# Kernel optimization log

Measured on AMD Instinct MI355X. Metric: run time of the kernel, lower is better.

The kernel has to match this reference:

```python
import jax, jax.numpy as jnp
import numpy as np


def _consts(n_fft):
    # Static index/twiddle tables, mirroring FastIMDCT4.__init__ (numpy, host-side).
    N4 = n_fft // 4
    k = np.arange(N4)
    pre0 = 2 * k                       # even taps
    pre1 = n_fft // 2 - 1 - 2 * k      # reversed odd taps
    tw = np.exp(-2j * np.pi / n_fft * (k.astype(np.float32) + 0.125)).astype(np.complex64)
    # post-FFT de-interleave index (length n_fft, values in [0, n_fft//2))
    idx = np.empty(n_fft, np.int64)
    idx[0:n_fft // 2:2] = np.arange(0, n_fft // 2, 2)
    idx[1:n_fft // 2:2] = np.arange(n_fft // 2 - 1, 0, -2)
    idx[n_fft // 2:] = idx[:n_fft // 2][::-1]
    post = np.roll(idx, -n_fft // 4)
    # sign pattern folded into the window
    sign = np.ones(n_fft, np.float64)
    sign[1::2] *= -1.0
    sign[:n_fft // 4] *= -1.0
    sign = np.roll(sign, -n_fft // 4)
    return pre0, pre1, tw, post, sign


def setup_inputs() -> dict:
    key = jax.random.key(0)
    B, T, n_fft, hop = 32, 1024, 2048, 1024
    signal = jax.random.normal(key, (B, T, n_fft // 2), dtype=jnp.float32)
    window = jnp.ones((n_fft,), dtype=jnp.float32)  # raw window (module default: ones)
    return {"signal": signal, "window": window, "n_fft": n_fft, "hop_length": hop}


def reference(signal, window, n_fft, hop_length):
    pre0, pre1, tw, post, sign = _consts(n_fft)
    # combined window: 4 * sign * window / n_fft (module precomputes this in __init__)
    win = (4.0 * jnp.asarray(sign, jnp.float32) * window / n_fft)
    # pre-twiddle gather -> complex [B, T, n_fft//4]
    c = signal[..., pre0] + 1j * signal[..., pre1]
    twj = jnp.asarray(tw)
    c = twj * c
    c = jnp.fft.fft(c, axis=-1)
    c = twj * c
    B, T = c.shape[0], c.shape[1]
    # interleave real/imag -> [B, T, n_fft//2], then post gather -> [B, T, n_fft]
    inter = jnp.stack([jnp.real(c), jnp.imag(c)], axis=-1).reshape(B, T, n_fft // 2)
    frames = win * inter[..., post]            # [B, T, n_fft]
    # overlap-add fold (F.fold with kernel (1, n_fft), stride (1, hop))
    out_len = (T - 1) * hop_length + n_fft
    pos = (np.arange(T)[:, None] * hop_length + np.arange(n_fft)[None, :]).reshape(-1)
    out = jnp.zeros((B, out_len), frames.dtype).at[:, pos].add(frames.reshape(B, -1))
    # center=True trimming
    out = out[:, n_fft // 2: -(n_fft // 2)]
    return out[:, None, None, :]               # [B, 1, 1, (T-1)*hop], matches fold output layout
```

## Files before the change

### kernel.cpp

```cpp
#include <hip/hip_runtime.h>


#define CHUNKS 1023

__device__ __forceinline__ float2 cmul(float2 a, float2 b) {
    return make_float2(a.x * b.x - a.y * b.y, a.x * b.y + a.y * b.x);
}
__device__ __forceinline__ float2 cadd(float2 a, float2 b) {
    return make_float2(a.x + b.x, a.y + b.y);
}
__device__ __forceinline__ float2 csub(float2 a, float2 b) {
    return make_float2(a.x - b.x, a.y - b.y);
}
__device__ __forceinline__ float2 twid(float rev) {
    return make_float2(__builtin_amdgcn_cosf(rev), __builtin_amdgcn_sinf(rev));
}

__device__ __forceinline__ void postmap(int m, int& p, float& sgn) {
    bool even = ((m & 1) == 0);
    if (m < 512)       p = even ? (m + 512)  : (512 - m);
    else if (m < 1536) p = even ? (m - 511)  : (1535 - m);
    else               p = even ? (m - 1536) : (2560 - m);
    float s1 = even ? 1.0f : -1.0f;
    sgn = (m < 1536) ? s1 : -s1;
}

__device__ __forceinline__ int brev3(int r) {
    return ((r & 1) << 2) | (r & 2) | ((r >> 2) & 1);
}

__device__ __forceinline__ void fft_frame(const float* __restrict__ row, int lane,
                                          float* __restrict__ planes) {
    const float2* row2 = (const float2*)row;
    const int rlane = (int)(__brev((unsigned)lane) >> 26);

    float2 v[8];
    #pragma unroll
    for (int r = 0; r < 8; ++r) v[r] = row2[64 * r + rlane];

    float2 c[8];
    #pragma unroll
    for (int r = 0; r < 8; ++r) {
        float im = __shfl_xor(v[7 - r].y, 63);
        int k = 64 * r + rlane;
        float rev = -((float)k + 0.125f) * (1.0f / 2048.0f);
        c[r] = cmul(twid(rev), make_float2(v[r].x, im));
    }

    const float RH = 0.70710678118654752f;
    {
        float2 u0 = c[0], u1 = c[1], u2 = c[2], u3 = c[3];
        float2 l0 = c[4], l1 = c[5], l2 = c[6], l3 = c[7];
        float2 t1 = csub(u1, l1), t2 = csub(u2, l2), t3 = csub(u3, l3);
        c[0] = cadd(u0, l0); c[4] = csub(u0, l0);
        c[1] = cadd(u1, l1); c[5] = cmul(make_float2(RH, -RH), t1);
        c[2] = cadd(u2, l2); c[6] = make_float2(t2.y, -t2.x);
        c[3] = cadd(u3, l3); c[7] = cmul(make_float2(-RH, -RH), t3);
    }
    #pragma unroll
    for (int b = 0; b < 8; b += 4) {
        float2 u0 = c[b], u1 = c[b + 1], d0 = c[b + 2], d1 = c[b + 3];
        float2 t = csub(u1, d1);
        c[b] = cadd(u0, d0);
        c[b + 2] = csub(u0, d0);
        c[b + 1] = cadd(u1, d1);
        c[b + 3] = make_float2(t.y, -t.x);
    }
    #pragma unroll
    for (int b = 0; b < 8; b += 2) {
        float2 u = c[b], d = c[b + 1];
        c[b] = cadd(u, d); c[b + 1] = csub(u, d);
    }

    #pragma unroll
    for (int r = 1; r < 8; ++r) {
        int k1 = brev3(r);
        float rev = -(float)(rlane * k1) * (1.0f / 512.0f);
        c[r] = cmul(twid(rev), c[r]);
    }

    #pragma unroll
    for (int s = 1; s <= 6; ++s) {
        const int half = 1 << (s - 1);
        const bool hi = (lane & half) != 0;
        float rev = -(float)(lane & (half - 1)) / (float)(1 << s);
        float2 w = twid(rev);
        #pragma unroll
        for (int r = 0; r < 8; ++r) {
            float ox = __shfl_xor(c[r].x, half);
            float oy = __shfl_xor(c[r].y, half);
            float2 oth = make_float2(ox, oy);
            if (s == 1) {
                c[r] = hi ? csub(oth, c[r]) : cadd(c[r], oth);
            } else {
                float2 t = cmul(w, hi ? c[r] : oth);
                c[r] = hi ? csub(oth, t) : cadd(c[r], t);
            }
        }
    }

    float2 d[8];
    #pragma unroll
    for (int j = 0; j < 8; ++j) {
        int r = brev3(j);
        int k = j + 8 * lane;
        float rev = -((float)k + 0.125f) * (1.0f / 2048.0f);
        d[j] = cmul(twid(rev), c[r]);
    }
    float4 r0 = make_float4(d[0].x, d[1].x, d[2].x, d[3].x);
    float4 r1 = make_float4(d[4].x, d[5].x, d[6].x, d[7].x);
    float4 i0 = make_float4(d[0].y, d[1].y, d[2].y, d[3].y);
    float4 i1 = make_float4(d[4].y, d[5].y, d[6].y, d[7].y);
    *(float4*)(planes + 8 * lane)           = r0;
    *(float4*)(planes + 8 * lane + 4)       = r1;
    *(float4*)(planes + 512 + 8 * lane)     = i0;
    *(float4*)(planes + 512 + 8 * lane + 4) = i1;
}

__global__ __launch_bounds__(256) void imdct_kernel(
        const float* __restrict__ signal,
        const float* __restrict__ window,
        float* __restrict__ out) {
    __shared__ float lds[4][2][2 * 512];

    const int tid = threadIdx.x;
    const int lane = tid & 63;
    const int w = tid >> 6;

    const int bid = blockIdx.x;
    const int nb = (bid & 7) * 1023 + (bid >> 3);
    const int chunk = nb * 4 + w;
    const int b = chunk / CHUNKS;
    const int q = chunk - b * CHUNKS;

    const float* base = signal + (size_t)(b * 1024 + q) * 1024;
    fft_frame(base,        lane, &lds[w][0][0]);
    fft_frame(base + 1024, lane, &lds[w][1][0]);

    const float* f0 = &lds[w][0][0];
    const float* f1 = &lds[w][1][0];
    float* orow = out + (size_t)b * (CHUNKS * 1024) + (size_t)q * 1024;

    #pragma unroll
    for (int it = 0; it < 4; ++it) {
        const int rbase = 256 * it + 4 * lane;
        float4 w_hi = *(const float4*)(window + 1024 + rbase);
        float4 w_lo = *(const float4*)(window + rbase);
        const float* whp = &w_hi.x;
        const float* wlp = &w_lo.x;
        float4 o;
        float* op = &o.x;
        #pragma unroll
        for (int e = 0; e < 4; ++e) {
            int r = rbase + e;
            int p0; float s0; postmap(1024 + r, p0, s0);
            int p1; float s1; postmap(r, p1, s1);
            float v0 = f0[(p0 & 1) * 512 + (p0 >> 1)];
            float v1 = f1[(p1 & 1) * 512 + (p1 >> 1)];
            op[e] = (s0 * whp[e] * v0 + s1 * wlp[e] * v1) * (1.0f / 512.0f);
        }
        *(float4*)(orow + rbase) = o;
    }
}

extern "C" void kernel_launch(void* const* d_in, const int* in_sizes, int n_in,
                              void* d_out, int out_size, void* d_ws, size_t ws_size,
                              hipStream_t stream) {
    const float* signal = (const float*)d_in[0];
    const float* window = (const float*)d_in[1];
    float* out = (float*)d_out;
    imdct_kernel<<<dim3(32 * CHUNKS / 4), dim3(256), 0, stream>>>(signal, window, out);
}
```

Measured before the change: 279.0 us.

## Share frame FFTs across output chunks in 512-thread blocks

Previously each wave computed two frame FFTs for one output chunk, so every frame's FFT was done twice. Now each 8-wave block computes 8 consecutive frames into LDS once, synchronises, and then writes 7 overlap-add output chunks that read adjacent frames. This roughly halves the FFT work, at the cost of a block-wide barrier, one idle FFT slot at the tail, and narrower float2 stores.

```diff
diff --git a/kernel.cpp b/kernel.cpp
--- a/kernel.cpp
+++ b/kernel.cpp
@@ -2,6 +2,8 @@
 
 
 #define CHUNKS 1023
+#define CPB 7
+#define BPB 147
 
 __device__ __forceinline__ float2 cmul(float2 a, float2 b) {
     return make_float2(a.x * b.x - a.y * b.y, a.x * b.y + a.y * b.x);
@@ -117,49 +119,51 @@
     *(float4*)(planes + 512 + 8 * lane + 4) = i1;
 }
 
-__global__ __launch_bounds__(256) void imdct_kernel(
+__global__ __launch_bounds__(512) void imdct_kernel(
         const float* __restrict__ signal,
         const float* __restrict__ window,
         float* __restrict__ out) {
-    __shared__ float lds[4][2][2 * 512];
+    __shared__ float lds[8][1024];
 
     const int tid = threadIdx.x;
     const int lane = tid & 63;
     const int w = tid >> 6;
 
     const int bid = blockIdx.x;
-    const int nb = (bid & 7) * 1023 + (bid >> 3);
-    const int chunk = nb * 4 + w;
-    const int b = chunk / CHUNKS;
-    const int q = chunk - b * CHUNKS;
+    const int b = bid / BPB;
+    const int cblk = bid - b * BPB;
+    const int q0 = cblk * CPB;
 
-    const float* base = signal + (size_t)(b * 1024 + q) * 1024;
-    fft_frame(base,        lane, &lds[w][0][0]);
-    fft_frame(base + 1024, lane, &lds[w][1][0]);
+    const int f = q0 + w;
+    if (f <= 1023) {
+        fft_frame(signal + (size_t)(b * 1024 + f) * 1024, lane, &lds[w][0]);
+    }
+    __syncthreads();
 
-    const float* f0 = &lds[w][0][0];
-    const float* f1 = &lds[w][1][0];
-    float* orow = out + (size_t)b * (CHUNKS * 1024) + (size_t)q * 1024;
+    float* orow_base = out + (size_t)b * (CHUNKS * 1024);
+    const int r = 2 * tid;
 
     #pragma unroll
-    for (int it = 0; it < 4; ++it) {
-        const int rbase = 256 * it + 4 * lane;
-        float4 w_hi = *(const float4*)(window + 1024 + rbase);
-        float4 w_lo = *(const float4*)(window + rbase);
-        const float* whp = &w_hi.x;
-        const float* wlp = &w_lo.x;
-        float4 o;
+    for (int j = 0; j < CPB; ++j) {
+        const int qj = q0 + j;
+        if (qj > 1022) break;
+        const float* f0 = &lds[j][0];
+        const float* f1 = &lds[j + 1][0];
+        float2 wh = *(const float2*)(window + 1024 + r);
+        float2 wl = *(const float2*)(window + r);
+        const float* whp = &wh.x;
+        const float* wlp = &wl.x;
+        float2 o;
         float* op = &o.x;
         #pragma unroll
-        for (int e = 0; e < 4; ++e) {
-            int r = rbase + e;
-            int p0; float s0; postmap(1024 + r, p0, s0);
-            int p1; float s1; postmap(r, p1, s1);
+        for (int e = 0; e < 2; ++e) {
+            int p0; float s0; postmap(1024 + r + e, p0, s0);
+            int p1; float s1; postmap(r + e, p1, s1);
             float v0 = f0[(p0 & 1) * 512 + (p0 >> 1)];
             float v1 = f1[(p1 & 1) * 512 + (p1 >> 1)];
             op[e] = (s0 * whp[e] * v0 + s1 * wlp[e] * v1) * (1.0f / 512.0f);
         }
-        *(float4*)(orow + rbase) = o;
+        *(float2*)(orow_base + (size_t)qj * 1024 + r) = o;
     }
 }
 
@@ -169,5 +173,5 @@
     const float* signal = (const float*)d_in[0];
     const float* window = (const float*)d_in[1];
     float* out = (float*)d_out;
-    imdct_kernel<<<dim3(32 * CHUNKS / 4), dim3(256), 0, stream>>>(signal, window, out);
+    imdct_kernel<<<dim3(32 * BPB), dim3(512), 0, stream>>>(signal, window, out);
 }
```

Measured after the change: 238.8 us. -14.4%, faster.
